# Kernel optimization log

Hardware: AMD Instinct MI355X
Metric: run time of the kernel (lower is better)

## Reference

```python
import jax, jax.numpy as jnp
import numpy as np
from jax import lax

GAMMA = 1.0       # SoftDTW gamma (init default)
MAX_DIST = 10000.0  # clamp in SoftDTW.forward
# bandwidth=None -> 0 -> Sakoe-Chiba pruning disabled (condition 0 < bandwidth never holds)


def _softdtw(D, gamma):
    """Soft-DTW DP via anti-diagonal wavefront scan. D: (B, N, M) -> (B,)."""
    B, N, M = D.shape
    R = jnp.full((B, N + 2, M + 2), jnp.inf, D.dtype).at[:, 0, 0].set(0.0)
    i_vec = jnp.arange(1, N + 1)  # row indices of interior cells

    def step(R, p):
        # cells on anti-diagonal p satisfy i + j == p + 2
        j_vec = p + 2 - i_vec
        valid = (j_vec >= 1) & (j_vec <= M)
        jc = jnp.clip(j_vec, 1, M)
        r0 = R[:, i_vec - 1, jc - 1]  # (B, N) diag
        r1 = R[:, i_vec - 1, jc]      # up
        r2 = R[:, i_vec, jc - 1]      # left
        neg = jnp.stack([r0, r1, r2], axis=0) * (-1.0 / gamma)  # (3, B, N)
        # invalid lanes: keep finite to avoid NaNs (result discarded by where)
        neg = jnp.where(valid[None, None, :], neg, 0.0)
        softmin = -gamma * jax.scipy.special.logsumexp(neg, axis=0)  # (B, N)
        new = D[:, i_vec - 1, jc - 1] + softmin
        R = R.at[:, i_vec, jc].set(jnp.where(valid[None, :], new, R[:, i_vec, jc]))
        return R, None

    R, _ = lax.scan(step, R, jnp.arange(N + M - 1))
    return R[:, N, M]


def setup_inputs() -> dict:
    key = jax.random.key(0)
    kx, ky = jax.random.split(key)
    X = jax.random.normal(kx, (16, 512, 64), dtype=jnp.float32)
    Y = jax.random.normal(ky, (16, 512, 64), dtype=jnp.float32)
    return {"X": X, "Y": Y}


def reference(X, Y):
    # squared Euclidean pairwise distance per timestep (faithful expand form)
    D = jnp.sum((X[:, :, None, :] - Y[:, None, :, :]) ** 2, axis=-1)  # (B, N, M)
    D = jnp.minimum(D, MAX_DIST)
    return _softdtw(D, GAMMA)
```

## Files before the change

kernel.cpp:

```cpp
#include <hip/hip_runtime.h>

#define BIGF 1e30f
#define LOG2E 1.4426950408889634f
#define LN2F 0.6931471805599453f

constexpr int NB = 16;
constexpr int NN = 512;
constexpr int MM = 512;
constexpr int KD = 64;
constexpr int WAVES = 8;
constexpr int CSPAN = 32;
constexpr int NSPANS = 32;
constexpr int SPW = 18;
constexpr int TPH = 3 * (WAVES - 1) + SPW;
constexpr int DIAGELEMS = NN * MM;

constexpr int BBSTRIDE = MM + 2;
constexpr int BUFD_FLOATS = WAVES * 2 * CSPAN * 64;
constexpr int BBUF_FLOATS = WAVES * BBSTRIDE;
constexpr int SMEM_BYTES = (BUFD_FLOATS + BBUF_FLOATS) * 4;

__device__ __forceinline__ int Bclosed(int s) {
  return (s <= 511) ? (s * (s + 1)) / 2
                    : DIAGELEMS - ((1023 - s) * (1024 - s)) / 2 - (s - 511);
}

__global__ __launch_bounds__(256) void pairdist_kernel(
    const float* __restrict__ X, const float* __restrict__ Y,
    float* __restrict__ Dsk) {
  const int b = blockIdx.z;
  const int i0 = blockIdx.y * 64;
  const int j0 = blockIdx.x * 64;

  __shared__ float Xs[64][65];
  __shared__ float Ys[64][65];
  __shared__ float Ds[64][66];

  const float* Xb = X + ((size_t)b * NN + i0) * KD;
  const float* Yb = Y + ((size_t)b * MM + j0) * KD;
  for (int k = threadIdx.x; k < 64 * KD; k += 256) {
    Xs[k >> 6][k & 63] = Xb[k];
    Ys[k >> 6][k & 63] = Yb[k];
  }
  __syncthreads();

  const int tx = threadIdx.x & 15;
  const int ty = threadIdx.x >> 4;
  const int r0 = ty * 4, c0 = tx * 4;

  float acc[4][4];
#pragma unroll
  for (int a = 0; a < 4; ++a)
#pragma unroll
    for (int e = 0; e < 4; ++e) acc[a][e] = 0.0f;

  for (int d = 0; d < KD; ++d) {
    float xv[4], yv[4];
#pragma unroll
    for (int q = 0; q < 4; ++q) xv[q] = Xs[r0 + q][d];
#pragma unroll
    for (int q = 0; q < 4; ++q) yv[q] = Ys[c0 + q][d];
#pragma unroll
    for (int a = 0; a < 4; ++a)
#pragma unroll
      for (int e = 0; e < 4; ++e) {
        float df = xv[a] - yv[e];
        acc[a][e] = fmaf(df, df, acc[a][e]);
      }
  }

#pragma unroll
  for (int a = 0; a < 4; ++a)
#pragma unroll
    for (int e = 0; e < 4; ++e)
      Ds[r0 + a][c0 + e] = fminf(acc[a][e], 10000.0f) * LOG2E;
  __syncthreads();

  const int wv = threadIdx.x >> 6;
  const int ln = threadIdx.x & 63;
  float* Db = Dsk + (size_t)b * DIAGELEMS;
  for (int sl = wv; sl < 127; sl += 4) {
    const int istart = sl > 63 ? sl - 63 : 0;
    const int iend = sl < 63 ? sl : 63;
    if (ln <= iend - istart) {
      const int ig = i0 + istart + ln;
      Db[Bclosed(i0 + j0 + sl) + ig] = Ds[istart + ln][sl - istart - ln];
    }
  }
}

__device__ __forceinline__ float dpp_shr1(float v, float fill) {
  return __int_as_float(__builtin_amdgcn_update_dpp(
      __float_as_int(fill), __float_as_int(v), 0x138 , 0xf, 0xf,
      false));
}

__device__ __forceinline__ void dma_span(const float* __restrict__ Dskb,
                                         float* bufD, int blk, int q,
                                         int lane) {
  float* dst0 = bufD + (blk * 2 + (q & 1)) * (CSPAN * 64);
  const int rbase = 64 * blk + (lane & 15) * 4;
  const int sub = lane >> 4;
#pragma unroll
  for (int u = 0; u < 8; ++u) {
    int s = 32 * q + 4 * u + sub;
    s = s > 1022 ? 1022 : s;
    int e = Bclosed(s) + rbase;
    e = e > DIAGELEMS - 4 ? DIAGELEMS - 4 : e;
    __builtin_amdgcn_global_load_lds(
        (const __attribute__((address_space(1))) void*)(Dskb + e),
        (__attribute__((address_space(3))) void*)(dst0 + u * 256), 16, 0, 0);
  }
}

extern __shared__ float smem[];
__global__ __launch_bounds__(512) void softdtw_kernel(
    const float* __restrict__ Dsk, float* __restrict__ out) {
  const int b = blockIdx.x;
  const int t = threadIdx.x;
  const int wu = __builtin_amdgcn_readfirstlane(t >> 6);
  const int lane = t & 63;
  const int blk = ((wu & 3) << 1) | (wu >> 2);

  float* bufD = smem;
  float* bbuf = smem + BUFD_FLOATS;

  for (int k = t; k < BBUF_FLOATS; k += 512) bbuf[k] = BIGF;
  __syncthreads();

  const float* __restrict__ Dskb = Dsk + (size_t)b * DIAGELEMS;

  dma_span(Dskb, bufD, blk, 2 * blk, lane);

  const int r = 64 * blk + lane;
  float ra = BIGF;
  float up1p = (blk == 0 && lane == 0) ? 0.0f : BIGF;

  for (int S = 0; S < TPH; ++S) {
    const int cc = S - 3 * blk;
    if (cc >= 0 && cc < SPW) {
      const int c = cc + 2 * blk;
      const bool issue = (cc + 1 < SPW);
      if (issue) {
        dma_span(Dskb, bufD, blk, c + 1, lane);
        asm volatile("s_waitcnt vmcnt(8)" ::: "memory");
      } else {
        asm volatile("s_waitcnt vmcnt(0)" ::: "memory");
      }

      int bi = 32 * cc + 1 + (lane & 31);
      bi = bi > 513 ? 513 : bi;
      const float browA = blk ? bbuf[blk * BBSTRIDE + bi] : BIGF;

      const float* myD = bufD + (blk * 2 + (c & 1)) * (CSPAN * 64);
      float dv[CSPAN];
#pragma unroll
      for (int k = 0; k < CSPAN; ++k) dv[k] = myD[k * 64 + lane];

      const int jv0 = 32 * c - r + 1;
#pragma unroll
      for (int k = 0; k < CSPAN; ++k) {
        const float o1 = __int_as_float(
            __builtin_amdgcn_readlane(__float_as_int(browA), k));
        const float up1 = dpp_shr1(ra, o1);
        const float up2 = up1p;
        up1p = up1;

        const float m = fminf(fminf(up1, up2), ra);
        const float md = __builtin_amdgcn_fmed3f(up1, up2, ra);
        const float mx = fmaxf(fmaxf(up1, up2), ra);
        const float ssum = 1.0f + __builtin_amdgcn_exp2f(m - md) +
                           __builtin_amdgcn_exp2f(m - mx);
        const float n = dv[k] + (m - __builtin_amdgcn_logf(ssum));

        const int jv = jv0 + k;
        const bool a0 = (unsigned)(jv - 1) < (unsigned)MM;
        ra = a0 ? n : ra;

        if (blk < WAVES - 1 && lane == 63 && a0)
          bbuf[(blk + 1) * BBSTRIDE + jv] = n;
      }
    }
    __syncthreads();
  }

  if (blk == WAVES - 1 && lane == 63) out[b] = ra * LN2F;
}

extern "C" void kernel_launch(void* const* d_in, const int* in_sizes, int n_in,
                              void* d_out, int out_size, void* d_ws,
                              size_t ws_size, hipStream_t stream) {
  const float* X = (const float*)d_in[0];
  const float* Y = (const float*)d_in[1];
  float* out = (float*)d_out;
  float* Dsk = (float*)d_ws;

  const size_t needed = (size_t)NB * DIAGELEMS * sizeof(float);
  if (ws_size < needed) return;

  hipFuncSetAttribute((const void*)softdtw_kernel,
                      hipFuncAttributeMaxDynamicSharedMemorySize, SMEM_BYTES);

  pairdist_kernel<<<dim3(MM / 64, NN / 64, NB), 256, 0, stream>>>(X, Y, Dsk);
  softdtw_kernel<<<NB, 512, SMEM_BYTES, stream>>>(Dsk, out);
}
```

Before: 148.9 us.

## Carry soft-DTW recurrence in linear mantissa/exponent domain instead of log-sum-exp

The soft-DTW DP now stores each cell as exp2(-R) split into a float mantissa and an integer exponent, so the softmin becomes scaled additions and one multiply in place of two exp2 calls and a log per cell. The pairdist kernel precomputes exp2 of the fractional part of D as fp16 packed with the integer part, and the mantissa is renormalised with frexp every four steps. D loads now go straight from global memory into registers with double-buffered prefetch, replacing the LDS DMA staging. The boundary row is passed through LDS as mantissa/exponent pairs written by every lane, not only lane 63. This trades transcendental latency on the serial critical path for ldexp/integer max work, and adds fp16 rounding of the D factor plus range risk from skipping renormalisation between steps.

```diff
diff --git a/kernel.cpp b/kernel.cpp
--- a/kernel.cpp
+++ b/kernel.cpp
@@ -1,6 +1,5 @@
 #include <hip/hip_runtime.h>
 
-#define BIGF 1e30f
 #define LOG2E 1.4426950408889634f
 #define LN2F 0.6931471805599453f
 
@@ -14,11 +13,10 @@
 constexpr int SPW = 18;
 constexpr int TPH = 3 * (WAVES - 1) + SPW;
 constexpr int DIAGELEMS = NN * MM;
-
-constexpr int BBSTRIDE = MM + 2;
-constexpr int BUFD_FLOATS = WAVES * 2 * CSPAN * 64;
-constexpr int BBUF_FLOATS = WAVES * BBSTRIDE;
-constexpr int SMEM_BYTES = (BUFD_FLOATS + BBUF_FLOATS) * 4;
+constexpr int EMIN = -(1 << 27);
+
+constexpr int BBPAD = 62;
+constexpr int BBSTRIDE = 648;
 
 __device__ __forceinline__ int Bclosed(int s) {
   return (s <= 511) ? (s * (s + 1)) / 2
@@ -27,7 +25,7 @@
 
 __global__ __launch_bounds__(256) void pairdist_kernel(
     const float* __restrict__ X, const float* __restrict__ Y,
-    float* __restrict__ Dsk) {
+    unsigned* __restrict__ Dsk) {
   const int b = blockIdx.z;
   const int i0 = blockIdx.y * 64;
   const int j0 = blockIdx.x * 64;
@@ -78,113 +76,134 @@
 
   const int wv = threadIdx.x >> 6;
   const int ln = threadIdx.x & 63;
-  float* Db = Dsk + (size_t)b * DIAGELEMS;
+  unsigned* Db = Dsk + (size_t)b * DIAGELEMS;
   for (int sl = wv; sl < 127; sl += 4) {
     const int istart = sl > 63 ? sl - 63 : 0;
     const int iend = sl < 63 ? sl : 63;
     if (ln <= iend - istart) {
       const int ig = i0 + istart + ln;
-      Db[Bclosed(i0 + j0 + sl) + ig] = Ds[istart + ln][sl - istart - ln];
+      const float Dp = Ds[istart + ln][sl - istart - ln];
+      const float ef = floorf(Dp);
+      const float mt = __builtin_amdgcn_exp2f(ef - Dp);
+      const unsigned short mh =
+          __builtin_bit_cast(unsigned short, (_Float16)mt);
+      Db[Bclosed(i0 + j0 + sl) + ig] = ((unsigned)(int)ef << 16) | mh;
     }
   }
 }
 
-__device__ __forceinline__ float dpp_shr1(float v, float fill) {
-  return __int_as_float(__builtin_amdgcn_update_dpp(
-      __float_as_int(fill), __float_as_int(v), 0x138 , 0xf, 0xf,
-      false));
-}
-
-__device__ __forceinline__ void dma_span(const float* __restrict__ Dskb,
-                                         float* bufD, int blk, int q,
-                                         int lane) {
-  float* dst0 = bufD + (blk * 2 + (q & 1)) * (CSPAN * 64);
-  const int rbase = 64 * blk + (lane & 15) * 4;
-  const int sub = lane >> 4;
-#pragma unroll
-  for (int u = 0; u < 8; ++u) {
-    int s = 32 * q + 4 * u + sub;
-    s = s > 1022 ? 1022 : s;
-    int e = Bclosed(s) + rbase;
-    e = e > DIAGELEMS - 4 ? DIAGELEMS - 4 : e;
-    __builtin_amdgcn_global_load_lds(
-        (const __attribute__((address_space(1))) void*)(Dskb + e),
-        (__attribute__((address_space(3))) void*)(dst0 + u * 256), 16, 0, 0);
-  }
-}
-
-extern __shared__ float smem[];
+__device__ __forceinline__ int dpp_shr1_old_i(int oldv, int v) {
+  return __builtin_amdgcn_update_dpp(oldv, v, 0x138, 0xf, 0xf, false);
+}
+__device__ __forceinline__ int dpp_shl1_i(int v) {
+  return __builtin_amdgcn_update_dpp(v, v, 0x130, 0xf, 0xf, false);
+}
+
 __global__ __launch_bounds__(512) void softdtw_kernel(
-    const float* __restrict__ Dsk, float* __restrict__ out) {
+    const unsigned* __restrict__ Dsk, float* __restrict__ out) {
   const int b = blockIdx.x;
   const int t = threadIdx.x;
   const int wu = __builtin_amdgcn_readfirstlane(t >> 6);
   const int lane = t & 63;
   const int blk = ((wu & 3) << 1) | (wu >> 2);
 
-  float* bufD = smem;
-  float* bbuf = smem + BUFD_FLOATS;
-
-  for (int k = t; k < BBUF_FLOATS; k += 512) bbuf[k] = BIGF;
+  __shared__ float2 bbuf[WAVES][BBSTRIDE];
+
+  for (int k = t; k < WAVES * BBSTRIDE; k += 512)
+    (&bbuf[0][0])[k] = make_float2(0.0f, __int_as_float(EMIN));
   __syncthreads();
 
-  const float* __restrict__ Dskb = Dsk + (size_t)b * DIAGELEMS;
-
-  dma_span(Dskb, bufD, blk, 2 * blk, lane);
-
+  const unsigned* __restrict__ Du = Dsk + (size_t)b * DIAGELEMS;
   const int r = 64 * blk + lane;
-  float ra = BIGF;
-  float up1p = (blk == 0 && lane == 0) ? 0.0f : BIGF;
+
+  float ma = 0.0f;  int ea = EMIN;
+  float u2m; int u2e;
+  if (blk == 0 && lane == 0) { u2m = 1.0f; u2e = 0; }
+  else { u2m = 0.0f; u2e = EMIN; }
+
+  unsigned dvA[CSPAN], dvB[CSPAN];
+
+#define FILL(ARR, Q)                                           \
+  do {                                                         \
+    const int q_ = (Q);                                        \
+    _Pragma("unroll") for (int k_ = 0; k_ < CSPAN; ++k_) {     \
+      int s_ = 32 * q_ + k_;                                   \
+      s_ = s_ > 1022 ? 1022 : s_;                              \
+      int e_ = Bclosed(s_) + r;                                \
+      e_ = e_ > DIAGELEMS - 1 ? DIAGELEMS - 1 : e_;            \
+      ARR[k_] = Du[e_];                                        \
+    }                                                          \
+  } while (0)
+
+#define STEP_CORE(PK)                                                   \
+  int u1m_i = dpp_shr1_old_i(__float_as_int(Bm), __float_as_int(ma));   \
+  int u1e = dpp_shr1_old_i(Be, ea);                                     \
+  Bm = __int_as_float(dpp_shl1_i(__float_as_int(Bm)));                  \
+  Be = dpp_shl1_i(Be);                                                  \
+  const float u1m = __int_as_float(u1m_i);                              \
+  const float mt =                                                      \
+      (float)__builtin_bit_cast(_Float16, (unsigned short)((PK)&0xffffu)); \
+  const int et = (int)((PK) >> 16);                                     \
+  int emax = max(max(u1e, u2e), ea);                                    \
+  float ssum = ldexpf(u1m, u1e - emax) + ldexpf(u2m, u2e - emax) +      \
+               ldexpf(ma, ea - emax);                                   \
+  float mraw = ssum * mt;                                               \
+  int eraw = emax - et;                                                 \
+  u2m = u1m;                                                            \
+  u2e = u1e;
+
+#define PHASE(DVC, DVN)                                                 \
+  do {                                                                  \
+    if (cc + 1 < SPW) FILL(DVN, c + 1);                                 \
+    __builtin_amdgcn_sched_barrier(0);                                  \
+    float Bm; int Be;                                                   \
+    if (blk) {                                                          \
+      int bi = BBPAD + 32 * cc + 1 + lane;                              \
+      bi = bi > BBSTRIDE - 1 ? BBSTRIDE - 1 : bi;                       \
+      const float2 Bv = bbuf[blk][bi];                                  \
+      Bm = Bv.x; Be = __float_as_int(Bv.y);                             \
+    } else {                                                            \
+      Bm = 0.0f; Be = EMIN;                                             \
+    }                                                                   \
+    float2* pubp = &bbuf[(blk + 1) & 7][BBPAD + 32 * c - r + 1];        \
+    if (cc >= 2 && cc <= 15) {       \
+      _Pragma("unroll") for (int k = 0; k < CSPAN; ++k) {               \
+        STEP_CORE(DVC[k]);                                              \
+        if ((k & 3) == 3) { int ex_; mraw = frexpf(mraw, &ex_); eraw += ex_; } \
+        ma = mraw; ea = eraw;                                           \
+        pubp[k] = make_float2(ma, __int_as_float(ea));                  \
+      }                                                                 \
+    } else {                    \
+      const int jv0 = 32 * c - r + 1;                                   \
+      _Pragma("unroll") for (int k = 0; k < CSPAN; ++k) {               \
+        STEP_CORE(DVC[k]);                                              \
+        if ((k & 3) == 3) { int ex_; mraw = frexpf(mraw, &ex_); eraw += ex_; } \
+        const bool a0 = (unsigned)(jv0 + k - 1) < (unsigned)MM;         \
+        ma = a0 ? mraw : ma;                                            \
+        ea = a0 ? eraw : ea;                                            \
+        pubp[k] = make_float2(ma, __int_as_float(ea));                  \
+      }                                                                 \
+    }                                                                   \
+  } while (0)
+
+  FILL(dvA, 2 * blk);
+  __builtin_amdgcn_sched_barrier(0);
 
   for (int S = 0; S < TPH; ++S) {
     const int cc = S - 3 * blk;
     if (cc >= 0 && cc < SPW) {
       const int c = cc + 2 * blk;
-      const bool issue = (cc + 1 < SPW);
-      if (issue) {
-        dma_span(Dskb, bufD, blk, c + 1, lane);
-        asm volatile("s_waitcnt vmcnt(8)" ::: "memory");
+      if (cc & 1) {
+        PHASE(dvB, dvA);
       } else {
-        asm volatile("s_waitcnt vmcnt(0)" ::: "memory");
-      }
-
-      int bi = 32 * cc + 1 + (lane & 31);
-      bi = bi > 513 ? 513 : bi;
-      const float browA = blk ? bbuf[blk * BBSTRIDE + bi] : BIGF;
-
-      const float* myD = bufD + (blk * 2 + (c & 1)) * (CSPAN * 64);
-      float dv[CSPAN];
-#pragma unroll
-      for (int k = 0; k < CSPAN; ++k) dv[k] = myD[k * 64 + lane];
-
-      const int jv0 = 32 * c - r + 1;
-#pragma unroll
-      for (int k = 0; k < CSPAN; ++k) {
-        const float o1 = __int_as_float(
-            __builtin_amdgcn_readlane(__float_as_int(browA), k));
-        const float up1 = dpp_shr1(ra, o1);
-        const float up2 = up1p;
-        up1p = up1;
-
-        const float m = fminf(fminf(up1, up2), ra);
-        const float md = __builtin_amdgcn_fmed3f(up1, up2, ra);
-        const float mx = fmaxf(fmaxf(up1, up2), ra);
-        const float ssum = 1.0f + __builtin_amdgcn_exp2f(m - md) +
-                           __builtin_amdgcn_exp2f(m - mx);
-        const float n = dv[k] + (m - __builtin_amdgcn_logf(ssum));
-
-        const int jv = jv0 + k;
-        const bool a0 = (unsigned)(jv - 1) < (unsigned)MM;
-        ra = a0 ? n : ra;
-
-        if (blk < WAVES - 1 && lane == 63 && a0)
-          bbuf[(blk + 1) * BBSTRIDE + jv] = n;
+        PHASE(dvA, dvB);
       }
     }
     __syncthreads();
   }
 
-  if (blk == WAVES - 1 && lane == 63) out[b] = ra * LN2F;
+  if (blk == WAVES - 1 && lane == 63)
+    out[b] = -(__builtin_amdgcn_logf(ma) + (float)ea) * LN2F;
 }
 
 extern "C" void kernel_launch(void* const* d_in, const int* in_sizes, int n_in,
@@ -193,14 +212,11 @@
   const float* X = (const float*)d_in[0];
   const float* Y = (const float*)d_in[1];
   float* out = (float*)d_out;
-  float* Dsk = (float*)d_ws;
-
-  const size_t needed = (size_t)NB * DIAGELEMS * sizeof(float);
+  unsigned* Dsk = (unsigned*)d_ws;
+
+  const size_t needed = (size_t)NB * DIAGELEMS * sizeof(unsigned);
   if (ws_size < needed) return;
 
-  hipFuncSetAttribute((const void*)softdtw_kernel,
-                      hipFuncAttributeMaxDynamicSharedMemorySize, SMEM_BYTES);
-
   pairdist_kernel<<<dim3(MM / 64, NN / 64, NB), 256, 0, stream>>>(X, Y, Dsk);
-  softdtw_kernel<<<NB, 512, SMEM_BYTES, stream>>>(Dsk, out);
-}
+  softdtw_kernel<<<NB, 512, 0, stream>>>(Dsk, out);
+}
```

New measurement: 182.7 us. 22.7% more time.
